# Optimization experiments

Hardware: AMD Instinct MI355X
Metric: run time of the kernel (lower is better)

The kernel has to match this reference:

```python
import jax, jax.numpy as jnp
import numpy as np

D_MODEL = 1024
NUM_HEADS = 16
BATCH = 4
SEQ = 2048


def _trunc_normal(key, shape, std):
    # truncated normal in [-3*std, 3*std], matching nn.init.trunc_normal_
    return jax.random.truncated_normal(key, -3.0, 3.0, shape, dtype=jnp.float32) * std


def setup_inputs() -> dict:
    key = jax.random.key(0)
    kx, kq, kk, kv, ko = jax.random.split(key, 5)
    std = np.sqrt(2.0 / (D_MODEL + D_MODEL)).astype(np.float32)
    x = jax.random.normal(kx, (BATCH, SEQ, D_MODEL), dtype=jnp.float32)
    # nn.Linear stores weight as [out, in]; y = x @ W.T
    W_q = _trunc_normal(kq, (D_MODEL, D_MODEL), std)
    W_k = _trunc_normal(kk, (D_MODEL, D_MODEL), std)
    W_v = _trunc_normal(kv, (D_MODEL, D_MODEL), std)
    W_o = _trunc_normal(ko, (D_MODEL, D_MODEL), std)
    return {"x": x, "W_q": W_q, "W_k": W_k, "W_v": W_v, "W_o": W_o}


def reference(x, W_q, W_k, W_v, W_o):
    b, s, d_model = x.shape
    h = NUM_HEADS
    d_k = d_model // h

    def split_heads(t):
        return t.reshape(b, s, h, d_k).transpose(0, 2, 1, 3)  # b h s d

    Q = split_heads(x @ W_q.T)
    K = split_heads(x @ W_k.T)
    V = split_heads(x @ W_v.T)

    # F.scaled_dot_product_attention with attn_mask=None -> NON-causal
    scale = 1.0 / jnp.sqrt(jnp.asarray(d_k, dtype=x.dtype))
    scores = jnp.einsum('bhqd,bhkd->bhqk', Q, K) * scale
    attn = jax.nn.softmax(scores, axis=-1)
    out = jnp.einsum('bhqk,bhkd->bhqd', attn, V)
    out = out.transpose(0, 2, 1, 3).reshape(b, s, d_model)
    return out @ W_o.T
```

## Files before the change

kernel.cpp:

```cpp
#include <hip/hip_runtime.h>
#include <hip/hip_bf16.h>
#include <stdint.h>


#define D_MODEL 1024
#define NHEAD 16
#define BATCH 4
#define SEQ 2048
#define DK 64
#define MTOT (BATCH * SEQ)

typedef __attribute__((ext_vector_type(4))) float f32x4;
typedef __attribute__((ext_vector_type(16))) float f32x16;
typedef __attribute__((ext_vector_type(8))) __bf16 bf16x8;
typedef __attribute__((ext_vector_type(8))) unsigned short ushort8;
typedef __attribute__((ext_vector_type(4))) unsigned short us4;

static __device__ __forceinline__ unsigned short f2bf(float f) {
  union { float f; unsigned int u; } v;
  v.f = f;
  unsigned int r = v.u + (0x7fffu + ((v.u >> 16) & 1u));
  return (unsigned short)(r >> 16);
}

static __device__ __forceinline__ f32x4 mfma16(bf16x8 a, bf16x8 b, f32x4 c) {
  return __builtin_amdgcn_mfma_f32_16x16x32_bf16(a, b, c, 0, 0, 0);
}
static __device__ __forceinline__ f32x16 mfma32(bf16x8 a, bf16x8 b, f32x16 c) {
  return __builtin_amdgcn_mfma_f32_32x32x16_bf16(a, b, c, 0, 0, 0);
}

static __device__ __forceinline__ unsigned int cvt_pk_bf16(float lo, float hi) {
  unsigned int r;
  asm("v_cvt_pk_bf16_f32 %0, %1, %2" : "=v"(r) : "v"(lo), "v"(hi));
  return r;
}

static __device__ __forceinline__ void gl_lds16(const void* g, void* l) {
  __builtin_amdgcn_global_load_lds((const __attribute__((address_space(1))) void*)g,
                                   (__attribute__((address_space(3))) void*)l, 16, 0, 0);
}

__global__ __launch_bounds__(256) void cvt_f32_bf16(const float* __restrict__ in,
                                                    unsigned short* __restrict__ out) {
  int i = blockIdx.x * 256 + threadIdx.x;
  f32x4 a = ((const f32x4*)in)[2 * i];
  f32x4 b = ((const f32x4*)in)[2 * i + 1];
  ushort8 r;
  r[0] = f2bf(a[0]); r[1] = f2bf(a[1]); r[2] = f2bf(a[2]); r[3] = f2bf(a[3]);
  r[4] = f2bf(b[0]); r[5] = f2bf(b[1]); r[6] = f2bf(b[2]); r[7] = f2bf(b[3]);
  ((ushort8*)out)[i] = r;
}

__global__ __launch_bounds__(256, 2) void gemm_qkv(const unsigned short* __restrict__ A,
                                                   const unsigned short* __restrict__ B3,
                                                   unsigned short* __restrict__ qh,
                                                   unsigned short* __restrict__ kh,
                                                   unsigned short* __restrict__ vtg,
                                                   float qscale) {
  __shared__ unsigned short lA[128][64];
  __shared__ unsigned short lB[128][64];
  const int t = threadIdx.x;
  const int wid = t >> 6, lane = t & 63;
  const int lr = lane & 15, lg = lane >> 4;
  const int wr = wid >> 1, wc = wid & 1;
  const int m0 = blockIdx.y * 128, n0 = blockIdx.x * 128;
  const int row8 = t >> 3, c8 = t & 7;

  f32x4 acc[4][4] = {};

  for (int kt = 0; kt < 16; ++kt) {
    const int k0 = kt * 64;
    if (kt) __syncthreads();
#pragma unroll
    for (int p = 0; p < 4; ++p) {
      gl_lds16(A  + (size_t)(m0 + p * 32 + row8) * 1024 + k0 + c8 * 8,
               &lA[0][0] + p * 2048 + t * 8);
      gl_lds16(B3 + (size_t)(n0 + p * 32 + row8) * 1024 + k0 + c8 * 8,
               &lB[0][0] + p * 2048 + t * 8);
    }
    __syncthreads();

    bf16x8 af[4][2], bfr[4][2];
#pragma unroll
    for (int rb = 0; rb < 4; ++rb)
#pragma unroll
      for (int kb = 0; kb < 2; ++kb) {
        af[rb][kb] = *(const bf16x8*)&lA[wr * 64 + rb * 16 + lr][kb * 32 + lg * 8];
        bfr[rb][kb] = *(const bf16x8*)&lB[wc * 64 + rb * 16 + lr][kb * 32 + lg * 8];
      }
    __builtin_amdgcn_s_setprio(1);
#pragma unroll
    for (int rb = 0; rb < 4; ++rb)
#pragma unroll
      for (int cb = 0; cb < 4; ++cb)
#pragma unroll
        for (int kb = 0; kb < 2; ++kb)
          acc[rb][cb] = mfma16(af[rb][kb], bfr[cb][kb], acc[rb][cb]);
    __builtin_amdgcn_s_setprio(0);
  }

  const int sel = n0 >> 10;
  const float scale = (sel == 0) ? qscale : 1.0f;
#pragma unroll
  for (int rb = 0; rb < 4; ++rb) {
    int mbase = m0 + wr * 64 + rb * 16 + lg * 4;
    int b = mbase >> 11, s0 = mbase & 2047;
#pragma unroll
    for (int cb = 0; cb < 4; ++cb) {
      int n = n0 + wc * 64 + cb * 16 + lr;
      int nl = n & 1023;
      int h = nl >> 6, d = nl & 63;
      if (sel == 2) {
        us4 v;
#pragma unroll
        for (int j = 0; j < 4; ++j) v[j] = f2bf(acc[rb][cb][j]);
        *(us4*)(vtg + ((size_t)(b * NHEAD + h) * DK + d) * SEQ + s0) = v;
      } else {
        unsigned short* out = (sel == 0) ? qh : kh;
#pragma unroll
        for (int j = 0; j < 4; ++j)
          out[((size_t)(b * NHEAD + h) * SEQ + s0 + j) * DK + d] = f2bf(acc[rb][cb][j] * scale);
      }
    }
  }
}

__global__ __launch_bounds__(256, 2) void gemm_o(const unsigned short* __restrict__ A,
                                                 const unsigned short* __restrict__ B,
                                                 float* __restrict__ out) {
  __shared__ unsigned short lA[128][64];
  __shared__ unsigned short lB[128][64];
  const int t = threadIdx.x;
  const int wid = t >> 6, lane = t & 63;
  const int lr = lane & 15, lg = lane >> 4;
  const int wr = wid >> 1, wc = wid & 1;
  const int m0 = blockIdx.y * 128, n0 = blockIdx.x * 128;
  const int row8 = t >> 3, c8 = t & 7;

  f32x4 acc[4][4] = {};

  for (int kt = 0; kt < 16; ++kt) {
    const int k0 = kt * 64;
    if (kt) __syncthreads();
#pragma unroll
    for (int p = 0; p < 4; ++p) {
      gl_lds16(A + (size_t)(m0 + p * 32 + row8) * 1024 + k0 + c8 * 8,
               &lA[0][0] + p * 2048 + t * 8);
      gl_lds16(B + (size_t)(n0 + p * 32 + row8) * 1024 + k0 + c8 * 8,
               &lB[0][0] + p * 2048 + t * 8);
    }
    __syncthreads();

    bf16x8 af[4][2], bfr[4][2];
#pragma unroll
    for (int rb = 0; rb < 4; ++rb)
#pragma unroll
      for (int kb = 0; kb < 2; ++kb) {
        af[rb][kb] = *(const bf16x8*)&lA[wr * 64 + rb * 16 + lr][kb * 32 + lg * 8];
        bfr[rb][kb] = *(const bf16x8*)&lB[wc * 64 + rb * 16 + lr][kb * 32 + lg * 8];
      }
    __builtin_amdgcn_s_setprio(1);
#pragma unroll
    for (int rb = 0; rb < 4; ++rb)
#pragma unroll
      for (int cb = 0; cb < 4; ++cb)
#pragma unroll
        for (int kb = 0; kb < 2; ++kb)
          acc[rb][cb] = mfma16(af[rb][kb], bfr[cb][kb], acc[rb][cb]);
    __builtin_amdgcn_s_setprio(0);
  }

#pragma unroll
  for (int rb = 0; rb < 4; ++rb) {
    int mbase = m0 + wr * 64 + rb * 16 + lg * 4;
#pragma unroll
    for (int cb = 0; cb < 4; ++cb) {
      int n = n0 + wc * 64 + cb * 16 + lr;
#pragma unroll
      for (int j = 0; j < 4; ++j)
        out[(size_t)(mbase + j) * 1024 + n] = acc[rb][cb][j];
    }
  }
}

__global__ __launch_bounds__(256, 3) void attn_fwd(const unsigned short* __restrict__ Qh,
                                                   const unsigned short* __restrict__ Kh,
                                                   const unsigned short* __restrict__ Vt_g,
                                                   unsigned short* __restrict__ Oout) {
  __shared__ unsigned short Kl[64 * 64];
  __shared__ unsigned short Vl[64 * 64];
  __shared__ unsigned short Ol[4][32][72];

  const int t = threadIdx.x;
  const int wq = t >> 6, lane = t & 63;
  const int l31 = lane & 31, hi = lane >> 5;

  const int wg = blockIdx.x;
  const int work = (wg & 7) * 128 + (wg >> 3);
  const int bh = work >> 4, qi = work & 15;
  const int q0 = qi * 128 + wq * 32;
  const size_t base = (size_t)bh * SEQ * DK;
  const int srow = t >> 3, sc = t & 7;

  bf16x8 qf[4];
#pragma unroll
  for (int dt = 0; dt < 4; ++dt)
    qf[dt] = *(const bf16x8*)(Qh + base + (size_t)(q0 + l31) * DK + dt * 16 + hi * 8);

  f32x16 o[2] = {};
  float l_run = 0.f;

  ushort8 rk0 = *(const ushort8*)(Kh + base + (size_t)srow * DK + sc * 8);
  ushort8 rk1 = *(const ushort8*)(Kh + base + (size_t)(srow + 32) * DK + sc * 8);
  ushort8 rv0 = *(const ushort8*)(Vt_g + base + (size_t)srow * SEQ + sc * 8);
  ushort8 rv1 = *(const ushort8*)(Vt_g + base + (size_t)(srow + 32) * SEQ + sc * 8);

  for (int kt = 0; kt < SEQ / 64; ++kt) {
    __syncthreads();
    {
      const int r0 = srow, r1 = srow + 32;
      *(ushort8*)((char*)Kl + ((r0 * 128 + sc * 16) ^ ((r0 & 7) << 4))) = rk0;
      *(ushort8*)((char*)Kl + ((r1 * 128 + sc * 16) ^ ((r1 & 7) << 4))) = rk1;
      *(ushort8*)((char*)Vl + ((r0 * 128 + sc * 16) ^ ((r0 & 7) << 4))) = rv0;
      *(ushort8*)((char*)Vl + ((r1 * 128 + sc * 16) ^ ((r1 & 7) << 4))) = rv1;
    }
    __syncthreads();

    if (kt < SEQ / 64 - 1) {
      const int nxt = (kt + 1) * 64;
      rk0 = *(const ushort8*)(Kh + base + (size_t)(nxt + srow) * DK + sc * 8);
      rk1 = *(const ushort8*)(Kh + base + (size_t)(nxt + srow + 32) * DK + sc * 8);
      rv0 = *(const ushort8*)(Vt_g + base + (size_t)srow * SEQ + nxt + sc * 8);
      rv1 = *(const ushort8*)(Vt_g + base + (size_t)(srow + 32) * SEQ + nxt + sc * 8);
    }

    f32x16 sS[2] = {};
    __builtin_amdgcn_s_setprio(1);
#pragma unroll
    for (int kb = 0; kb < 2; ++kb) {
      const int row = kb * 32 + l31;
#pragma unroll
      for (int dt = 0; dt < 4; ++dt) {
        bf16x8 kf = *(const bf16x8*)((const char*)Kl +
                      ((row * 128 + dt * 32 + hi * 16) ^ ((row & 7) << 4)));
        sS[kb] = mfma32(kf, qf[dt], sS[kb]);
      }
    }
    __builtin_amdgcn_s_setprio(0);

    float s0 = 0.f, s1 = 0.f, s2 = 0.f, s3 = 0.f;
#pragma unroll
    for (int kb = 0; kb < 2; ++kb)
#pragma unroll
      for (int r = 0; r < 16; r += 4) {
        float p0 = __builtin_amdgcn_exp2f(sS[kb][r + 0]);
        float p1 = __builtin_amdgcn_exp2f(sS[kb][r + 1]);
        float p2 = __builtin_amdgcn_exp2f(sS[kb][r + 2]);
        float p3 = __builtin_amdgcn_exp2f(sS[kb][r + 3]);
        sS[kb][r + 0] = p0; sS[kb][r + 1] = p1;
        sS[kb][r + 2] = p2; sS[kb][r + 3] = p3;
        s0 += p0; s1 += p1; s2 += p2; s3 += p3;
      }
    float psum = (s0 + s1) + (s2 + s3);
    psum += __shfl_xor(psum, 32, 64);
    l_run += psum;

    __builtin_amdgcn_s_setprio(1);
#pragma unroll
    for (int ks = 0; ks < 4; ++ks) {
      const int kk = ks >> 1, rb = (ks & 1) * 8;
      unsigned int a0 = cvt_pk_bf16(sS[kk][rb + 0], sS[kk][rb + 1]);
      unsigned int a1 = cvt_pk_bf16(sS[kk][rb + 2], sS[kk][rb + 3]);
      unsigned int b0 = cvt_pk_bf16(sS[kk][rb + 4], sS[kk][rb + 5]);
      unsigned int b1 = cvt_pk_bf16(sS[kk][rb + 6], sS[kk][rb + 7]);
      asm("v_permlane32_swap_b32 %0, %1" : "+v"(a0), "+v"(b0));
      asm("v_permlane32_swap_b32 %0, %1" : "+v"(a1), "+v"(b1));
      union { unsigned int u[4]; bf16x8 v; } pw;
      pw.u[0] = a0; pw.u[1] = a1; pw.u[2] = b0; pw.u[3] = b1;
#pragma unroll
      for (int dt = 0; dt < 2; ++dt) {
        const int row = dt * 32 + l31;
        bf16x8 vf = *(const bf16x8*)((const char*)Vl +
                      ((row * 128 + ks * 32 + hi * 16) ^ ((row & 7) << 4)));
        o[dt] = mfma32(vf, pw.v, o[dt]);
      }
    }
    __builtin_amdgcn_s_setprio(0);
  }

  const float inv = 1.0f / l_run;
#pragma unroll
  for (int dt = 0; dt < 2; ++dt)
#pragma unroll
    for (int r = 0; r < 16; ++r) {
      const int d = dt * 32 + (r & 3) + 8 * (r >> 2) + 4 * hi;
      Ol[wq][l31][d] = f2bf(o[dt][r] * inv);
    }
  __syncthreads();
  const int b = bh >> 4, hh = bh & 15;
#pragma unroll
  for (int cc = 0; cc < 4; ++cc) {
    ushort8 v = *(const ushort8*)&Ol[wq][l31][hi * 32 + cc * 8];
    *(ushort8*)(Oout + (size_t)(b * SEQ + q0 + l31) * D_MODEL + hh * 64 + hi * 32 + cc * 8) = v;
  }
}

extern "C" void kernel_launch(void* const* d_in, const int* in_sizes, int n_in,
                              void* d_out, int out_size, void* d_ws, size_t ws_size,
                              hipStream_t stream) {
  (void)in_sizes; (void)n_in; (void)out_size; (void)ws_size;
  const float* x = (const float*)d_in[0];
  const float* Wq = (const float*)d_in[1];
  const float* Wk = (const float*)d_in[2];
  const float* Wv = (const float*)d_in[3];
  const float* Wo = (const float*)d_in[4];

  char* ws = (char*)d_ws;
  unsigned short* xb   = (unsigned short*)(ws + 0);
  unsigned short* wqkv = (unsigned short*)(ws + 16777216);
  unsigned short* wob  = (unsigned short*)(ws + 23068672);
  unsigned short* qh   = (unsigned short*)(ws + 25165824);
  unsigned short* kh   = (unsigned short*)(ws + 41943040);
  unsigned short* vtg  = (unsigned short*)(ws + 58720256);
  unsigned short* at   = (unsigned short*)(ws + 75497472);

  cvt_f32_bf16<<<4096, 256, 0, stream>>>(x, xb);
  cvt_f32_bf16<<<512, 256, 0, stream>>>(Wq, wqkv);
  cvt_f32_bf16<<<512, 256, 0, stream>>>(Wk, wqkv + 1048576);
  cvt_f32_bf16<<<512, 256, 0, stream>>>(Wv, wqkv + 2097152);
  cvt_f32_bf16<<<512, 256, 0, stream>>>(Wo, wob);

  gemm_qkv<<<dim3(24, 64), 256, 0, stream>>>(xb, wqkv, qh, kh, vtg, 0.1803368801f);

  attn_fwd<<<1024, 256, 0, stream>>>(qh, kh, vtg, at);

  gemm_o<<<dim3(8, 64), 256, 0, stream>>>(at, wob, (float*)d_out);
}
```

Measured before the change: 196.1 us.

## Split attention KV range into two halves and merge partial outputs

```diff
diff --git a/kernel.cpp b/kernel.cpp
--- a/kernel.cpp
+++ b/kernel.cpp
@@ -21,6 +21,11 @@
   v.f = f;
   unsigned int r = v.u + (0x7fffu + ((v.u >> 16) & 1u));
   return (unsigned short)(r >> 16);
+}
+static __device__ __forceinline__ float bf2f(unsigned short u) {
+  union { unsigned int u; float f; } v;
+  v.u = (unsigned int)u << 16;
+  return v.f;
 }
 
 static __device__ __forceinline__ f32x4 mfma16(bf16x8 a, bf16x8 b, f32x4 c) {
@@ -187,21 +192,25 @@
 __global__ __launch_bounds__(256, 3) void attn_fwd(const unsigned short* __restrict__ Qh,
                                                    const unsigned short* __restrict__ Kh,
                                                    const unsigned short* __restrict__ Vt_g,
-                                                   unsigned short* __restrict__ Oout) {
+                                                   unsigned short* __restrict__ P0,
+                                                   unsigned short* __restrict__ P1,
+                                                   float* __restrict__ Lb) {
   __shared__ unsigned short Kl[64 * 64];
   __shared__ unsigned short Vl[64 * 64];
-  __shared__ unsigned short Ol[4][32][72];
 
   const int t = threadIdx.x;
   const int wq = t >> 6, lane = t & 63;
   const int l31 = lane & 31, hi = lane >> 5;
 
   const int wg = blockIdx.x;
-  const int work = (wg & 7) * 128 + (wg >> 3);
-  const int bh = work >> 4, qi = work & 15;
+  const int work = (wg & 7) * 256 + (wg >> 3);
+  const int half = work >> 10;
+  const int bhq = work & 1023;
+  const int bh = bhq >> 4, qi = bhq & 15;
   const int q0 = qi * 128 + wq * 32;
   const size_t base = (size_t)bh * SEQ * DK;
   const int srow = t >> 3, sc = t & 7;
+  const int kvbase = half * 1024;
 
   bf16x8 qf[4];
 #pragma unroll
@@ -211,12 +220,12 @@
   f32x16 o[2] = {};
   float l_run = 0.f;
 
-  ushort8 rk0 = *(const ushort8*)(Kh + base + (size_t)srow * DK + sc * 8);
-  ushort8 rk1 = *(const ushort8*)(Kh + base + (size_t)(srow + 32) * DK + sc * 8);
-  ushort8 rv0 = *(const ushort8*)(Vt_g + base + (size_t)srow * SEQ + sc * 8);
-  ushort8 rv1 = *(const ushort8*)(Vt_g + base + (size_t)(srow + 32) * SEQ + sc * 8);
-
-  for (int kt = 0; kt < SEQ / 64; ++kt) {
+  ushort8 rk0 = *(const ushort8*)(Kh + base + (size_t)(kvbase + srow) * DK + sc * 8);
+  ushort8 rk1 = *(const ushort8*)(Kh + base + (size_t)(kvbase + srow + 32) * DK + sc * 8);
+  ushort8 rv0 = *(const ushort8*)(Vt_g + base + (size_t)srow * SEQ + kvbase + sc * 8);
+  ushort8 rv1 = *(const ushort8*)(Vt_g + base + (size_t)(srow + 32) * SEQ + kvbase + sc * 8);
+
+  for (int kt = 0; kt < 16; ++kt) {
     __syncthreads();
     {
       const int r0 = srow, r1 = srow + 32;
@@ -227,8 +236,8 @@
     }
     __syncthreads();
 
-    if (kt < SEQ / 64 - 1) {
-      const int nxt = (kt + 1) * 64;
+    if (kt < 15) {
+      const int nxt = kvbase + (kt + 1) * 64;
       rk0 = *(const ushort8*)(Kh + base + (size_t)(nxt + srow) * DK + sc * 8);
       rk1 = *(const ushort8*)(Kh + base + (size_t)(nxt + srow + 32) * DK + sc * 8);
       rv0 = *(const ushort8*)(Vt_g + base + (size_t)srow * SEQ + nxt + sc * 8);
@@ -289,21 +298,38 @@
     __builtin_amdgcn_s_setprio(0);
   }
 
-  const float inv = 1.0f / l_run;
+  const int b = bh >> 4, hh = bh & 15;
+  const int q = q0 + l31;
+  unsigned short* pat = half ? P1 : P0;
+  unsigned short* orow = pat + (size_t)(b * SEQ + q) * D_MODEL + hh * 64 + hi * 4;
 #pragma unroll
   for (int dt = 0; dt < 2; ++dt)
 #pragma unroll
-    for (int r = 0; r < 16; ++r) {
-      const int d = dt * 32 + (r & 3) + 8 * (r >> 2) + 4 * hi;
-      Ol[wq][l31][d] = f2bf(o[dt][r] * inv);
-    }
-  __syncthreads();
-  const int b = bh >> 4, hh = bh & 15;
-#pragma unroll
-  for (int cc = 0; cc < 4; ++cc) {
-    ushort8 v = *(const ushort8*)&Ol[wq][l31][hi * 32 + cc * 8];
-    *(ushort8*)(Oout + (size_t)(b * SEQ + q0 + l31) * D_MODEL + hh * 64 + hi * 32 + cc * 8) = v;
-  }
+    for (int i = 0; i < 4; ++i) {
+      us4 v;
+#pragma unroll
+      for (int j = 0; j < 4; ++j) v[j] = f2bf(o[dt][4 * i + j]);
+      *(us4*)(orow + dt * 32 + 8 * i) = v;
+    }
+  if (hi == 0) Lb[(size_t)(half * 64 + bh) * SEQ + q] = l_run;
+}
+
+__global__ __launch_bounds__(256) void merge_halves(unsigned short* __restrict__ p0,
+                                                    const unsigned short* __restrict__ p1,
+                                                    const float* __restrict__ Lb) {
+  const int tid = blockIdx.x * 256 + threadIdx.x;
+  const size_t e = (size_t)tid * 8;
+  const int h = (int)((e >> 6) & 15);
+  const int s = (int)((e >> 10) & 2047);
+  const int b = (int)(e >> 21);
+  const size_t li = (size_t)(b * NHEAD + h) * SEQ + s;
+  const float inv = 1.0f / (Lb[li] + Lb[(size_t)64 * SEQ + li]);
+  ushort8 a = *(const ushort8*)(p0 + e);
+  ushort8 c = *(const ushort8*)(p1 + e);
+  ushort8 r;
+#pragma unroll
+  for (int j = 0; j < 8; ++j) r[j] = f2bf((bf2f(a[j]) + bf2f(c[j])) * inv);
+  *(ushort8*)(p0 + e) = r;
 }
 
 extern "C" void kernel_launch(void* const* d_in, const int* in_sizes, int n_in,
@@ -325,6 +351,9 @@
   unsigned short* vtg  = (unsigned short*)(ws + 58720256);
   unsigned short* at   = (unsigned short*)(ws + 75497472);
 
+  unsigned short* p1 = xb;
+  float* lb = (float*)wqkv;
+
   cvt_f32_bf16<<<4096, 256, 0, stream>>>(x, xb);
   cvt_f32_bf16<<<512, 256, 0, stream>>>(Wq, wqkv);
   cvt_f32_bf16<<<512, 256, 0, stream>>>(Wk, wqkv + 1048576);
@@ -333,7 +362,8 @@
 
   gemm_qkv<<<dim3(24, 64), 256, 0, stream>>>(xb, wqkv, qh, kh, vtg, 0.1803368801f);
 
-  attn_fwd<<<1024, 256, 0, stream>>>(qh, kh, vtg, at);
+  attn_fwd<<<2048, 256, 0, stream>>>(qh, kh, vtg, at, p1, lb);
+  merge_halves<<<4096, 256, 0, stream>>>(at, p1, lb);
 
   gemm_o<<<dim3(8, 64), 256, 0, stream>>>(at, wob, (float*)d_out);
 }
```

After: 204.5 us. 1.04x slower.

## Process two 32-row query tiles per wave in attention to reuse K/V loads

Applied to the files above, without the earlier changes.

```diff
diff --git a/kernel.cpp b/kernel.cpp
--- a/kernel.cpp
+++ b/kernel.cpp
@@ -184,32 +184,33 @@
   }
 }
 
-__global__ __launch_bounds__(256, 3) void attn_fwd(const unsigned short* __restrict__ Qh,
+__global__ __launch_bounds__(256, 2) void attn_fwd(const unsigned short* __restrict__ Qh,
                                                    const unsigned short* __restrict__ Kh,
                                                    const unsigned short* __restrict__ Vt_g,
                                                    unsigned short* __restrict__ Oout) {
   __shared__ unsigned short Kl[64 * 64];
   __shared__ unsigned short Vl[64 * 64];
-  __shared__ unsigned short Ol[4][32][72];
 
   const int t = threadIdx.x;
   const int wq = t >> 6, lane = t & 63;
   const int l31 = lane & 31, hi = lane >> 5;
 
   const int wg = blockIdx.x;
-  const int work = (wg & 7) * 128 + (wg >> 3);
-  const int bh = work >> 4, qi = work & 15;
-  const int q0 = qi * 128 + wq * 32;
+  const int work = (wg & 7) * 64 + (wg >> 3);
+  const int bh = work >> 3, qi = work & 7;
+  const int q0 = qi * 256 + wq * 64;
   const size_t base = (size_t)bh * SEQ * DK;
   const int srow = t >> 3, sc = t & 7;
 
-  bf16x8 qf[4];
-#pragma unroll
-  for (int dt = 0; dt < 4; ++dt)
-    qf[dt] = *(const bf16x8*)(Qh + base + (size_t)(q0 + l31) * DK + dt * 16 + hi * 8);
-
-  f32x16 o[2] = {};
-  float l_run = 0.f;
+  bf16x8 qf0[4], qf1[4];
+#pragma unroll
+  for (int dt = 0; dt < 4; ++dt) {
+    qf0[dt] = *(const bf16x8*)(Qh + base + (size_t)(q0 + l31) * DK + dt * 16 + hi * 8);
+    qf1[dt] = *(const bf16x8*)(Qh + base + (size_t)(q0 + 32 + l31) * DK + dt * 16 + hi * 8);
+  }
+
+  f32x16 o0[2] = {}, o1[2] = {};
+  float l0 = 0.f, l1 = 0.f;
 
   ushort8 rk0 = *(const ushort8*)(Kh + base + (size_t)srow * DK + sc * 8);
   ushort8 rk1 = *(const ushort8*)(Kh + base + (size_t)(srow + 32) * DK + sc * 8);
@@ -235,7 +236,7 @@
       rv1 = *(const ushort8*)(Vt_g + base + (size_t)(srow + 32) * SEQ + nxt + sc * 8);
     }
 
-    f32x16 sS[2] = {};
+    f32x16 sS0[2] = {}, sS1[2] = {};
     __builtin_amdgcn_s_setprio(1);
 #pragma unroll
     for (int kb = 0; kb < 2; ++kb) {
@@ -244,65 +245,111 @@
       for (int dt = 0; dt < 4; ++dt) {
         bf16x8 kf = *(const bf16x8*)((const char*)Kl +
                       ((row * 128 + dt * 32 + hi * 16) ^ ((row & 7) << 4)));
-        sS[kb] = mfma32(kf, qf[dt], sS[kb]);
+        sS0[kb] = mfma32(kf, qf0[dt], sS0[kb]);
+        sS1[kb] = mfma32(kf, qf1[dt], sS1[kb]);
       }
     }
     __builtin_amdgcn_s_setprio(0);
 
-    float s0 = 0.f, s1 = 0.f, s2 = 0.f, s3 = 0.f;
-#pragma unroll
-    for (int kb = 0; kb < 2; ++kb)
-#pragma unroll
-      for (int r = 0; r < 16; r += 4) {
-        float p0 = __builtin_amdgcn_exp2f(sS[kb][r + 0]);
-        float p1 = __builtin_amdgcn_exp2f(sS[kb][r + 1]);
-        float p2 = __builtin_amdgcn_exp2f(sS[kb][r + 2]);
-        float p3 = __builtin_amdgcn_exp2f(sS[kb][r + 3]);
-        sS[kb][r + 0] = p0; sS[kb][r + 1] = p1;
-        sS[kb][r + 2] = p2; sS[kb][r + 3] = p3;
-        s0 += p0; s1 += p1; s2 += p2; s3 += p3;
-      }
-    float psum = (s0 + s1) + (s2 + s3);
-    psum += __shfl_xor(psum, 32, 64);
-    l_run += psum;
+    {
+      float a0 = 0.f, a1 = 0.f, a2 = 0.f, a3 = 0.f;
+#pragma unroll
+      for (int kb = 0; kb < 2; ++kb)
+#pragma unroll
+        for (int r = 0; r < 16; r += 4) {
+          float p0 = __builtin_amdgcn_exp2f(sS0[kb][r + 0]);
+          float p1 = __builtin_amdgcn_exp2f(sS0[kb][r + 1]);
+          float p2 = __builtin_amdgcn_exp2f(sS0[kb][r + 2]);
+          float p3 = __builtin_amdgcn_exp2f(sS0[kb][r + 3]);
+          sS0[kb][r + 0] = p0; sS0[kb][r + 1] = p1;
+          sS0[kb][r + 2] = p2; sS0[kb][r + 3] = p3;
+          a0 += p0; a1 += p1; a2 += p2; a3 += p3;
+        }
+      float ps = (a0 + a1) + (a2 + a3);
+      ps += __shfl_xor(ps, 32, 64);
+      l0 += ps;
+    }
+    {
+      float a0 = 0.f, a1 = 0.f, a2 = 0.f, a3 = 0.f;
+#pragma unroll
+      for (int kb = 0; kb < 2; ++kb)
+#pragma unroll
+        for (int r = 0; r < 16; r += 4) {
+          float p0 = __builtin_amdgcn_exp2f(sS1[kb][r + 0]);
+          float p1 = __builtin_amdgcn_exp2f(sS1[kb][r + 1]);
+          float p2 = __builtin_amdgcn_exp2f(sS1[kb][r + 2]);
+          float p3 = __builtin_amdgcn_exp2f(sS1[kb][r + 3]);
+          sS1[kb][r + 0] = p0; sS1[kb][r + 1] = p1;
+          sS1[kb][r + 2] = p2; sS1[kb][r + 3] = p3;
+          a0 += p0; a1 += p1; a2 += p2; a3 += p3;
+        }
+      float ps = (a0 + a1) + (a2 + a3);
+      ps += __shfl_xor(ps, 32, 64);
+      l1 += ps;
+    }
 
     __builtin_amdgcn_s_setprio(1);
 #pragma unroll
     for (int ks = 0; ks < 4; ++ks) {
       const int kk = ks >> 1, rb = (ks & 1) * 8;
-      unsigned int a0 = cvt_pk_bf16(sS[kk][rb + 0], sS[kk][rb + 1]);
-      unsigned int a1 = cvt_pk_bf16(sS[kk][rb + 2], sS[kk][rb + 3]);
-      unsigned int b0 = cvt_pk_bf16(sS[kk][rb + 4], sS[kk][rb + 5]);
-      unsigned int b1 = cvt_pk_bf16(sS[kk][rb + 6], sS[kk][rb + 7]);
+      unsigned int a0 = cvt_pk_bf16(sS0[kk][rb + 0], sS0[kk][rb + 1]);
+      unsigned int a1 = cvt_pk_bf16(sS0[kk][rb + 2], sS0[kk][rb + 3]);
+      unsigned int b0 = cvt_pk_bf16(sS0[kk][rb + 4], sS0[kk][rb + 5]);
+      unsigned int b1 = cvt_pk_bf16(sS0[kk][rb + 6], sS0[kk][rb + 7]);
       asm("v_permlane32_swap_b32 %0, %1" : "+v"(a0), "+v"(b0));
       asm("v_permlane32_swap_b32 %0, %1" : "+v"(a1), "+v"(b1));
-      union { unsigned int u[4]; bf16x8 v; } pw;
-      pw.u[0] = a0; pw.u[1] = a1; pw.u[2] = b0; pw.u[3] = b1;
+      union { unsigned int u[4]; bf16x8 v; } pw0;
+      pw0.u[0] = a0; pw0.u[1] = a1; pw0.u[2] = b0; pw0.u[3] = b1;
+
+      unsigned int c0 = cvt_pk_bf16(sS1[kk][rb + 0], sS1[kk][rb + 1]);
+      unsigned int c1 = cvt_pk_bf16(sS1[kk][rb + 2], sS1[kk][rb + 3]);
+      unsigned int d0 = cvt_pk_bf16(sS1[kk][rb + 4], sS1[kk][rb + 5]);
+      unsigned int d1 = cvt_pk_bf16(sS1[kk][rb + 6], sS1[kk][rb + 7]);
+      asm("v_permlane32_swap_b32 %0, %1" : "+v"(c0), "+v"(d0));
+      asm("v_permlane32_swap_b32 %0, %1" : "+v"(c1), "+v"(d1));
+      union { unsigned int u[4]; bf16x8 v; } pw1;
+      pw1.u[0] = c0; pw1.u[1] = c1; pw1.u[2] = d0; pw1.u[3] = d1;
+
 #pragma unroll
       for (int dt = 0; dt < 2; ++dt) {
         const int row = dt * 32 + l31;
         bf16x8 vf = *(const bf16x8*)((const char*)Vl +
                       ((row * 128 + ks * 32 + hi * 16) ^ ((row & 7) << 4)));
-        o[dt] = mfma32(vf, pw.v, o[dt]);
+        o0[dt] = mfma32(vf, pw0.v, o0[dt]);
+        o1[dt] = mfma32(vf, pw1.v, o1[dt]);
       }
     }
     __builtin_amdgcn_s_setprio(0);
   }
 
-  const float inv = 1.0f / l_run;
-#pragma unroll
-  for (int dt = 0; dt < 2; ++dt)
-#pragma unroll
-    for (int r = 0; r < 16; ++r) {
-      const int d = dt * 32 + (r & 3) + 8 * (r >> 2) + 4 * hi;
-      Ol[wq][l31][d] = f2bf(o[dt][r] * inv);
-    }
-  __syncthreads();
   const int b = bh >> 4, hh = bh & 15;
-#pragma unroll
-  for (int cc = 0; cc < 4; ++cc) {
-    ushort8 v = *(const ushort8*)&Ol[wq][l31][hi * 32 + cc * 8];
-    *(ushort8*)(Oout + (size_t)(b * SEQ + q0 + l31) * D_MODEL + hh * 64 + hi * 32 + cc * 8) = v;
+  {
+    const int q = q0 + l31;
+    const float inv = 1.0f / l0;
+    unsigned short* orow = Oout + (size_t)(b * SEQ + q) * D_MODEL + hh * 64 + hi * 4;
+#pragma unroll
+    for (int dt = 0; dt < 2; ++dt)
+#pragma unroll
+      for (int i = 0; i < 4; ++i) {
+        us4 v;
+#pragma unroll
+        for (int j = 0; j < 4; ++j) v[j] = f2bf(o0[dt][4 * i + j] * inv);
+        *(us4*)(orow + dt * 32 + 8 * i) = v;
+      }
+  }
+  {
+    const int q = q0 + 32 + l31;
+    const float inv = 1.0f / l1;
+    unsigned short* orow = Oout + (size_t)(b * SEQ + q) * D_MODEL + hh * 64 + hi * 4;
+#pragma unroll
+    for (int dt = 0; dt < 2; ++dt)
+#pragma unroll
+      for (int i = 0; i < 4; ++i) {
+        us4 v;
+#pragma unroll
+        for (int j = 0; j < 4; ++j) v[j] = f2bf(o1[dt][4 * i + j] * inv);
+        *(us4*)(orow + dt * 32 + 8 * i) = v;
+      }
   }
 }
 
@@ -333,7 +380,7 @@
 
   gemm_qkv<<<dim3(24, 64), 256, 0, stream>>>(xb, wqkv, qh, kh, vtg, 0.1803368801f);
 
-  attn_fwd<<<1024, 256, 0, stream>>>(qh, kh, vtg, at);
+  attn_fwd<<<512, 256, 0, stream>>>(qh, kh, vtg, at);
 
   gemm_o<<<dim3(8, 64), 256, 0, stream>>>(at, wob, (float*)d_out);
 }
```

After: 188.2 us. 4.0% less time.
